# Kernel optimization log

Measured on AMD Instinct MI355X. Metric: run time of the kernel, lower is better.

Reference implementation:

```python
import jax, jax.numpy as jnp
import numpy as np

# ---- module hyperparameters (from init_kwargs) ----
DIST = 25
N_IN, N_HID, N_OUT = 16, 128, 2
D_MODEL, D_STATE, D_CONV, EXPAND, HEADDIM = 256, 64, 4, 2, 64
D_INNER = EXPAND * D_MODEL            # 512
NHEADS = D_INNER // HEADDIM           # 8
CONV_DIM = D_INNER + 2 * D_STATE      # 640 (x, B, C share the conv)
D_IN_PROJ = 2 * D_INNER + 2 * D_STATE + NHEADS  # 1160
NUM_CHECK = DIST ** 2 - 1             # 624 (mamba seq len)
NPG = NUM_CHECK + DIST ** 2           # 1249 nodes per graph
BATCH = 64
N_NODES = BATCH * NPG                 # 79936
N_EDGES = N_NODES * 8                 # 639488


def setup_inputs() -> dict:
    key = jax.random.key(0)
    ks = jax.random.split(key, 16)
    w = lambda k, shape, s=0.02: jax.random.normal(k, shape, jnp.float32) * s
    return {
        "node_inputs": jax.random.normal(ks[0], (N_NODES, N_IN), jnp.float32),
        "src_ids": jax.random.randint(ks[1], (N_EDGES,), 0, N_NODES),
        "dst_ids": jax.random.randint(ks[2], (N_EDGES,), 0, N_NODES),
        "W_embed": w(ks[3], (N_IN, D_MODEL)), "b_embed": jnp.zeros((D_MODEL,), jnp.float32),
        "W_in": w(ks[4], (D_MODEL, D_IN_PROJ)), "b_in": jnp.zeros((D_IN_PROJ,), jnp.float32),
        "conv_w": w(ks[5], (CONV_DIM, D_CONV), 0.1), "conv_b": jnp.zeros((CONV_DIM,), jnp.float32),
        "A_log": jnp.log(jnp.arange(1, NHEADS + 1, dtype=jnp.float32)),
        "dt_bias": w(ks[6], (NHEADS,), 0.1),
        "D_skip": jnp.ones((NHEADS,), jnp.float32),
        "norm_w": jnp.ones((D_INNER,), jnp.float32),
        "W_outp": w(ks[7], (D_INNER, D_MODEL)), "b_outp": jnp.zeros((D_MODEL,), jnp.float32),
        "W_proj": w(ks[8], (D_MODEL, N_IN)), "b_proj": jnp.zeros((N_IN,), jnp.float32),
        "W_msg": w(ks[9], (N_IN, N_HID)), "b_msg": jnp.zeros((N_HID,), jnp.float32),
        "W_upd": w(ks[10], (N_IN + N_HID, N_HID)), "b_upd": jnp.zeros((N_HID,), jnp.float32),
        "W_out": w(ks[11], (N_HID, N_OUT)), "b_out": jnp.zeros((N_OUT,), jnp.float32),
    }


def _silu(x):
    return x * jax.nn.sigmoid(x)


def _mamba2(x, W_in, b_in, conv_w, conv_b, A_log, dt_bias, D_skip, norm_w, W_outp, b_outp):
    """Mamba2 block: in_proj -> causal depthwise conv -> selective scan -> gated RMSNorm -> out_proj."""
    Bg, L, _ = x.shape
    zxbcdt = x @ W_in + b_in                       # [Bg, L, 1160]
    z = zxbcdt[..., :D_INNER]                      # gate
    xBC = zxbcdt[..., D_INNER:D_INNER + CONV_DIM]
    dt = zxbcdt[..., D_INNER + CONV_DIM:]          # [Bg, L, H]
    # causal depthwise conv over the seq dim (d_conv taps)
    xp = jnp.pad(xBC, ((0, 0), (D_CONV - 1, 0), (0, 0)))
    xBC = sum(conv_w[:, k] * xp[:, k:k + L, :] for k in range(D_CONV)) + conv_b
    xBC = _silu(xBC)
    xs = xBC[..., :D_INNER].reshape(Bg, L, NHEADS, HEADDIM)
    Bm = xBC[..., D_INNER:D_INNER + D_STATE]       # [Bg, L, N] (ngroups=1)
    Cm = xBC[..., D_INNER + D_STATE:]              # [Bg, L, N]
    dt = jax.nn.softplus(dt + dt_bias)             # [Bg, L, H]
    dA = jnp.exp(dt * (-jnp.exp(A_log)))           # [Bg, L, H]

    def step(h, inp):
        xt, Bt, Ct, dAt, dtt = inp                 # xt [Bg,H,P], Bt/Ct [Bg,N], dAt/dtt [Bg,H]
        h = dAt[..., None, None] * h + dtt[..., None, None] * xt[..., None] * Bt[:, None, None, :]
        yt = jnp.einsum('bhpn,bn->bhp', h, Ct)
        return h, yt

    h0 = jnp.zeros((Bg, NHEADS, HEADDIM, D_STATE), x.dtype)
    seq = (jnp.moveaxis(xs, 1, 0), jnp.moveaxis(Bm, 1, 0), jnp.moveaxis(Cm, 1, 0),
           jnp.moveaxis(dA, 1, 0), jnp.moveaxis(dt, 1, 0))
    _, ys = jax.lax.scan(step, h0, seq)
    ys = jnp.moveaxis(ys, 1, 0) + xs * D_skip[None, None, :, None]   # [Bg, L, H, P]
    y = ys.reshape(Bg, L, D_INNER) * _silu(z)                        # gated
    y = y * jax.lax.rsqrt(jnp.mean(y * y, axis=-1, keepdims=True) + 1e-5) * norm_w
    return y @ W_outp + b_outp


def reference(node_inputs, src_ids, dst_ids, W_embed, b_embed, W_in, b_in, conv_w, conv_b,
              A_log, dt_bias, D_skip, norm_w, W_outp, b_outp, W_proj, b_proj,
              W_msg, b_msg, W_upd, b_upd, W_out, b_out):
    # gather check-node rows: i*nodes_per_graph + j for j < num_check
    idx = (jnp.arange(BATCH)[:, None] * NPG + jnp.arange(NUM_CHECK)[None, :]).reshape(-1)
    chk = node_inputs[idx]                                           # [B*624, 16]
    emb = (chk @ W_embed + b_embed).reshape(BATCH, NUM_CHECK, D_MODEL)
    y = _mamba2(emb, W_in, b_in, conv_w, conv_b, A_log, dt_bias, D_skip, norm_w, W_outp, b_outp)
    proj = y.reshape(-1, D_MODEL) @ W_proj + b_proj                  # [B*624, 16]
    # scatter back into zero tensor at check-node slots
    feat = jnp.zeros((node_inputs.shape[0], N_IN), node_inputs.dtype).at[idx].set(proj)
    # GNN message passing: gather src, transform, scatter-sum into dst, update, readout
    msg = jax.nn.relu(feat[src_ids] @ W_msg + b_msg)                 # [E, n_hidden]
    agg = jax.ops.segment_sum(msg, dst_ids, num_segments=feat.shape[0])
    h = jax.nn.relu(jnp.concatenate([feat, agg], axis=-1) @ W_upd + b_upd)
    return h @ W_out + b_out                                         # [N, n_node_outputs]
```

## Files before the change

kernel.cpp:

```cpp
#include <hip/hip_runtime.h>
#include <math.h>

#define LSEQ 624
#define NPG_C 1249
#define BATCH_C 64
#define NROWS (BATCH_C*LSEQ)
#define N_NODES_C 79936
#define N_EDGES_C 639488
#define DIP 1160
#define DIN 512
#define CDIM 640
#define NH 8
#define HD 64
#define DS 64
#define CAP 96
#define TCH 48
#define NCHK 13
#define HSLOT 2097152

#define OFF_CHK   0
#define OFF_WF    638976
#define OFF_BF    657536
#define OFF_WOP   658944
#define OFF_BOP   667136
#define OFF_XBC   667392
#define OFF_DTV   26226432
#define OFF_EV    26545920
#define OFF_YS    26865408
#define OFF_FEAT  47312640
#define OFF_AGG   48591616
#define OFF_ECUM  (OFF_AGG + 2000000)
#define OFF_BBF   (OFF_AGG + 2400000)
#define OFF_PROJ  (OFF_XBC + 8000000)

typedef __attribute__((ext_vector_type(8))) short bf16x8;
typedef __attribute__((ext_vector_type(4))) float f32x4;

__device__ __forceinline__ float siluf(float x) {
    return x / (1.f + __expf(-x));
}

__device__ __forceinline__ unsigned short f2bf(float f) {
    unsigned int u = __float_as_uint(f);
    u += 0x7fffu + ((u >> 16) & 1u);
    return (unsigned short)(u >> 16);
}
__device__ __forceinline__ float bf2f(unsigned short h) {
    return __uint_as_float(((unsigned int)h) << 16);
}

__device__ __forceinline__ unsigned short* hstp(unsigned short* hst, int c, int b, int head) {
    return hst + (size_t)(c - 1) * HSLOT + (size_t)(b * NH + head) * 4096;
}

__global__ void k_gather(const float* __restrict__ ni, float* __restrict__ chk) {
    int gid = blockIdx.x * 256 + threadIdx.x;
    if (gid >= NROWS * 16) return;
    int row = gid >> 4, k = gid & 15;
    int node = (row / LSEQ) * NPG_C + (row % LSEQ);
    chk[gid] = ni[node * 16 + k];
}

__global__ void k_fusew(const float* __restrict__ We, const float* __restrict__ be,
                        const float* __restrict__ Wi, const float* __restrict__ bi,
                        const float* __restrict__ Wo, const float* __restrict__ bo,
                        const float* __restrict__ Wp, const float* __restrict__ bp,
                        float* __restrict__ Wf, float* __restrict__ bf,
                        float* __restrict__ Wop, float* __restrict__ bop) {
    int id = blockIdx.x * 256 + threadIdx.x;
    if (id < 16 * DIP) {
        int i = id / DIP, j = id % DIP;
        float s = 0.f;
        for (int k = 0; k < 256; k++) s = fmaf(We[i * 256 + k], Wi[k * DIP + j], s);
        Wf[id] = s;
    } else if (id < 16 * DIP + DIP) {
        int j = id - 16 * DIP;
        float s = bi[j];
        for (int k = 0; k < 256; k++) s = fmaf(be[k], Wi[k * DIP + j], s);
        bf[j] = s;
    } else if (id < 16 * DIP + DIP + DIN * 16) {
        int id2 = id - (16 * DIP + DIP);
        int c = id2 >> 4, o = id2 & 15;
        float s = 0.f;
        for (int k = 0; k < 256; k++) s = fmaf(Wo[c * 256 + k], Wp[k * 16 + o], s);
        Wop[id2] = s;
    } else if (id < 16 * DIP + DIP + DIN * 16 + 16) {
        int o = id - (16 * DIP + DIP + DIN * 16);
        float s = bp[o];
        for (int k = 0; k < 256; k++) s = fmaf(bo[k], Wp[k * 16 + o], s);
        bop[o] = s;
    }
}

__global__ __launch_bounds__(320) void k_conv(const float* __restrict__ chk,
        const float* __restrict__ Wf, const float* __restrict__ bf,
        const float* __restrict__ cw, const float* __restrict__ cb,
        float* __restrict__ xBCc, unsigned short* __restrict__ bbf) {
    int c = blockIdx.x * 320 + threadIdx.x;
    int t0 = blockIdx.y * 78;
    int b = blockIdx.z;
    float w[16];
#pragma unroll
    for (int k = 0; k < 16; k++) w[k] = Wf[k * DIP + DIN + c];
    float bfx = bf[DIN + c];
    float k0 = cw[c * 4 + 0], k1 = cw[c * 4 + 1], k2 = cw[c * 4 + 2], k3 = cw[c * 4 + 3];
    float cbv = cb[c];
    const float* crow = chk + (size_t)(b * LSEQ) * 16;
    float* out = xBCc + (size_t)(b * LSEQ) * CDIM + c;
    int isB = (c >= 512 && c < 576);
    unsigned short* bout = bbf + (size_t)(b * LSEQ) * 64 + (c - 512);

    float w0 = 0.f, w1 = 0.f, w2 = 0.f;
#pragma unroll
    for (int d = 3; d >= 1; d--) {
        int tau = t0 - d;
        float s = 0.f;
        if (tau >= 0) {
            s = bfx;
            const float* cr = crow + tau * 16;
#pragma unroll
            for (int k = 0; k < 16; k++) s = fmaf(cr[k], w[k], s);
        }
        if (d == 3) w0 = s; else if (d == 2) w1 = s; else w2 = s;
    }
    for (int t = t0; t < t0 + 78; t++) {
        const float* cr = crow + t * 16;
        float w3 = bfx;
#pragma unroll
        for (int k = 0; k < 16; k++) w3 = fmaf(cr[k], w[k], w3);
        float a = fmaf(k0, w0, fmaf(k1, w1, fmaf(k2, w2, fmaf(k3, w3, cbv))));
        float v = siluf(a);
        out[(size_t)t * CDIM] = v;
        if (isB) bout[(size_t)t * 64] = f2bf(v);
        w0 = w1; w1 = w2; w2 = w3;
    }
}

__global__ __launch_bounds__(256) void k_dte(const float* __restrict__ chk,
        const float* __restrict__ Wf, const float* __restrict__ bf,
        const float* __restrict__ A_log, const float* __restrict__ dt_bias,
        float* __restrict__ dtv, float* __restrict__ ecum) {
    int s = blockIdx.x * 4 + (threadIdx.x >> 6);
    int lane = threadIdx.x & 63;
    int h = s & 7;
    int cb = s >> 3;
    int c = cb % NCHK, b = cb / NCHK;
    int r0 = b * LSEQ + c * TCH;
    float wcol[16];
#pragma unroll
    for (int k = 0; k < 16; k++) wcol[k] = Wf[k * DIP + DIN + CDIM + h];
    float base = bf[DIN + CDIM + h] + dt_bias[h];
    float nA = -__expf(A_log[h]);
    float v = 0.f, sp = 0.f;
    if (lane < TCH) {
        const float* cr = chk + (size_t)(r0 + lane) * 16;
        float acc = base;
#pragma unroll
        for (int k = 0; k < 16; k++) acc = fmaf(cr[k], wcol[k], acc);
        sp = (acc > 20.f) ? acc : log1pf(__expf(acc));
        v = nA * sp;
    }
#pragma unroll
    for (int off = 1; off < 64; off <<= 1) {
        float u = __shfl_up(v, off);
        if (lane >= off) v += u;
    }
    if (lane < TCH) {
        dtv[(size_t)(r0 + lane) * NH + h] = sp;
        ecum[(size_t)(r0 + lane) * NH + h] = v;
    }
}

__global__ __launch_bounds__(256) void k_gmat(const float* __restrict__ xBCc,
        float* __restrict__ Gm) {
    int c = blockIdx.x, b = blockIdx.y;
    int tid = threadIdx.x;
    int bs = b * LSEQ;
    __shared__ __align__(16) float sBC[TCH * 132];
#pragma unroll
    for (int j = 0; j < 6; j++) {
        int g = j * 256 + tid;
        int f = g * 4;
        int t = f >> 7, col = f & 127;
        float4 v = *(const float4*)(xBCc + (size_t)(bs + c * TCH + t) * CDIM + 512 + col);
        *(float4*)&sBC[t * 132 + col] = v;
    }
    __syncthreads();
    int t0 = (tid >> 4) * 3, s0 = (tid & 15) * 3;
    float acc[3][3];
#pragma unroll
    for (int i = 0; i < 3; i++)
#pragma unroll
        for (int j = 0; j < 3; j++) acc[i][j] = 0.f;
    for (int k = 0; k < 64; k++) {
        float c0 = sBC[(t0 + 0) * 132 + 64 + k];
        float c1 = sBC[(t0 + 1) * 132 + 64 + k];
        float c2 = sBC[(t0 + 2) * 132 + 64 + k];
        float b0 = sBC[(s0 + 0) * 132 + k];
        float b1 = sBC[(s0 + 1) * 132 + k];
        float b2 = sBC[(s0 + 2) * 132 + k];
        acc[0][0] = fmaf(c0, b0, acc[0][0]); acc[0][1] = fmaf(c0, b1, acc[0][1]); acc[0][2] = fmaf(c0, b2, acc[0][2]);
        acc[1][0] = fmaf(c1, b0, acc[1][0]); acc[1][1] = fmaf(c1, b1, acc[1][1]); acc[1][2] = fmaf(c1, b2, acc[1][2]);
        acc[2][0] = fmaf(c2, b0, acc[2][0]); acc[2][1] = fmaf(c2, b1, acc[2][1]); acc[2][2] = fmaf(c2, b2, acc[2][2]);
    }
    size_t gb = (size_t)(b * NCHK + c) * (TCH * TCH);
#pragma unroll
    for (int i = 0; i < 3; i++)
#pragma unroll
        for (int j = 0; j < 3; j++)
            Gm[gb + (t0 + i) * TCH + (s0 + j)] = acc[i][j];
}

__global__ __launch_bounds__(256) void k_scarry(const float* __restrict__ xBCc,
        const unsigned short* __restrict__ bbf,
        const float* __restrict__ dtv, const float* __restrict__ ecum,
        unsigned short* __restrict__ hst) {
    int head = blockIdx.x, b = blockIdx.y;
    int pz = blockIdx.z * 32;
    int tid = threadIdx.x;
    int bs = b * LSEQ;
    __shared__ __align__(16) float sX[TCH * 32];
    __shared__ __align__(16) float sB[TCH * 64];
    __shared__ float sW[TCH];

    int i2 = (tid >> 4) * 2;
    int j4 = (tid & 15) * 4;

    float h[2][4];
#pragma unroll
    for (int i = 0; i < 2; i++)
#pragma unroll
        for (int j = 0; j < 4; j++) h[i][j] = 0.f;

    float4 rX0, rX1;
    ushort4 rBu[3];
    float rEc = 0.f, rDt = 0.f, rEcL = 0.f;

#define SC_ISSUE(cc)                                                                \
    {                                                                               \
        int r0i = bs + (cc) * TCH;                                                  \
        {   int f = 4 * tid; int t = f >> 5; int col = f & 31;                      \
            rX0 = *(const float4*)(xBCc + (size_t)(r0i + t) * CDIM + head * HD + pz + col); \
            if (tid < 128) {                                                        \
                int f2 = 1024 + 4 * tid; int t2 = f2 >> 5; int col2 = f2 & 31;      \
                rX1 = *(const float4*)(xBCc + (size_t)(r0i + t2) * CDIM + head * HD + pz + col2); \
            }                                                                       \
        }                                                                           \
        _Pragma("unroll")                                                           \
        for (int jj = 0; jj < 3; jj++) {                                            \
            int g = jj * 256 + tid; int f = 4 * g; int t = f >> 6; int col = f & 63;\
            rBu[jj] = *(const ushort4*)(bbf + (size_t)(r0i + t) * 64 + col);        \
        }                                                                           \
        if (tid < TCH) { rEc = ecum[(size_t)(r0i + tid) * NH + head];               \
                         rDt = dtv[(size_t)(r0i + tid) * NH + head]; }              \
        rEcL = ecum[(size_t)(r0i + TCH - 1) * NH + head];                           \
    }

    SC_ISSUE(0);
    for (int c = 0; c < NCHK; c++) {
        __syncthreads();
        float eL = __expf(rEcL);
        {
            int f = 4 * tid;
            *(float4*)&sX[f] = rX0;
            if (tid < 128) *(float4*)&sX[1024 + f] = rX1;
        }
#pragma unroll
        for (int jj = 0; jj < 3; jj++) {
            int g = jj * 256 + tid;
            float4 bv = { bf2f(rBu[jj].x), bf2f(rBu[jj].y), bf2f(rBu[jj].z), bf2f(rBu[jj].w) };
            *(float4*)&sB[4 * g] = bv;
        }
        if (tid < TCH) sW[tid] = __expf(rEcL - rEc) * rDt;
        __syncthreads();
        if (c + 1 < NCHK) SC_ISSUE(c + 1);

        if (c > 0) {
            unsigned short* hp = hstp(hst, c, b, head);
#pragma unroll
            for (int ii = 0; ii < 2; ii++) {
                ushort4 v = { f2bf(h[ii][0]), f2bf(h[ii][1]), f2bf(h[ii][2]), f2bf(h[ii][3]) };
                *(ushort4*)&hp[(pz + i2 + ii) * 64 + j4] = v;
            }
        }

#pragma unroll
        for (int i = 0; i < 2; i++)
#pragma unroll
            for (int j = 0; j < 4; j++) h[i][j] *= eL;
        for (int s = 0; s < TCH; s++) {
            float w = sW[s];
            float2 xv = *(const float2*)&sX[s * 32 + i2];
            float4 bv = *(const float4*)&sB[s * 64 + j4];
            float x0 = w * xv.x, x1 = w * xv.y;
            h[0][0] = fmaf(x0, bv.x, h[0][0]); h[0][1] = fmaf(x0, bv.y, h[0][1]);
            h[0][2] = fmaf(x0, bv.z, h[0][2]); h[0][3] = fmaf(x0, bv.w, h[0][3]);
            h[1][0] = fmaf(x1, bv.x, h[1][0]); h[1][1] = fmaf(x1, bv.y, h[1][1]);
            h[1][2] = fmaf(x1, bv.z, h[1][2]); h[1][3] = fmaf(x1, bv.w, h[1][3]);
        }
    }
#undef SC_ISSUE
}

__global__ __launch_bounds__(256) void k_intra(float* __restrict__ xBCc,
        const float* __restrict__ Gm, const float* __restrict__ dtv,
        const float* __restrict__ ecum, const float* __restrict__ Dskip,
        const unsigned short* __restrict__ hst) {
    int bid = blockIdx.x;
    int xcd = bid & 7;
    int head = (bid >> 3) & 7;
    int g = (bid >> 6) * 8 + xcd;
    int c = g % NCHK, b = g / NCHK;
    int tid = threadIdx.x;
    int lane = tid & 63;
    int wv = tid >> 6;
    int bs = b * LSEQ;
    int r0 = bs + c * TCH;

    __shared__ __align__(16) unsigned char smraw[52032];
    float* sXf = (float*)(smraw);
    unsigned short* sHt = (unsigned short*)(smraw);
    unsigned short* sCt = (unsigned short*)(smraw + 12288);
    unsigned short* sMh = (unsigned short*)(smraw + 19200);
    unsigned short* sMl = (unsigned short*)(smraw + 26112);
    unsigned short* sXh = (unsigned short*)(smraw + 33024);
    unsigned short* sXl = (unsigned short*)(smraw + 42240);
    float* sE  = (float*)(smraw + 51456);
    float* sEx = (float*)(smraw + 51648);
    float* sdt = (float*)(smraw + 51840);

    ushort4 rHu[4];
    if (c > 0) {
        const unsigned short* hp = hstp((unsigned short*)hst, c, b, head);
#pragma unroll
        for (int j = 0; j < 4; j++)
            rHu[j] = *(const ushort4*)(hp + 4 * (j * 256 + tid));
    }

#pragma unroll
    for (int j = 0; j < 3; j++) {
        int g2 = j * 256 + tid;
        int t = g2 >> 4, col = (g2 & 15) * 4;
        const float* rowp = xBCc + (size_t)(r0 + t) * CDIM;
        float4 xv = *(const float4*)(rowp + head * HD + col);
        *(float4*)&sXf[t * 64 + col] = xv;
        float4 cv = *(const float4*)(rowp + 576 + col);
        ushort4 cu = { f2bf(cv.x), f2bf(cv.y), f2bf(cv.z), f2bf(cv.w) };
        *(ushort4*)&sCt[t * 72 + col] = cu;
    }
    if (tid < TCH) {
        float e = ecum[(size_t)(r0 + tid) * NH + head];
        sE[tid] = e;
        sEx[tid] = __expf(e);
        sdt[tid] = dtv[(size_t)(r0 + tid) * NH + head];
    }
    __syncthreads();

    size_t gb = (size_t)(b * NCHK + c) * (TCH * TCH);
#pragma unroll
    for (int k = 0; k < 9; k++) {
        int id = k * 256 + tid;
        int t = id / TCH, s = id - t * TCH;
        float gv = Gm[gb + id];
        float m = (s <= t) ? __expf(sE[t] - sE[s]) * sdt[s] * gv : 0.f;
        unsigned short mh = f2bf(m);
        sMh[t * 72 + s] = mh;
        sMl[t * 72 + s] = f2bf(m - bf2f(mh));
    }
    for (int w = tid; w < 768; w += 256) {
        int t = w >> 4, s = 48 + (w & 15);
        sMh[t * 72 + s] = 0;
        sMl[t * 72 + s] = 0;
    }
#pragma unroll
    for (int i = 0; i < 3; i++) {
        int w = i * 256 + tid;
        int p = w & 63, k4 = (w >> 6) * 4;
        float v0 = sXf[(k4 + 0) * 64 + p];
        float v1 = sXf[(k4 + 1) * 64 + p];
        float v2 = sXf[(k4 + 2) * 64 + p];
        float v3 = sXf[(k4 + 3) * 64 + p];
        unsigned short h0 = f2bf(v0), h1 = f2bf(v1), h2 = f2bf(v2), h3 = f2bf(v3);
        ushort4 hi = { h0, h1, h2, h3 };
        ushort4 lo = { f2bf(v0 - bf2f(h0)), f2bf(v1 - bf2f(h1)),
                       f2bf(v2 - bf2f(h2)), f2bf(v3 - bf2f(h3)) };
        *(ushort4*)&sXh[p * 72 + k4] = hi;
        *(ushort4*)&sXl[p * 72 + k4] = lo;
    }
    {
        int p = tid >> 2, k4 = 48 + (tid & 3) * 4;
        ushort4 z = { 0, 0, 0, 0 };
        *(ushort4*)&sXh[p * 72 + k4] = z;
        *(ushort4*)&sXl[p * 72 + k4] = z;
    }
    __syncthreads();

    int pt = wv * 16;
    int colL = lane & 15;
    int rbase = (lane >> 4) * 4;
    int kfrag = 8 * (lane >> 4);

    float xo[3][4];
#pragma unroll
    for (int tt = 0; tt < 3; tt++)
#pragma unroll
        for (int r = 0; r < 4; r++)
            xo[tt][r] = sXf[(tt * 16 + rbase + r) * 64 + pt + colL];

    f32x4 acc[3] = { {0,0,0,0}, {0,0,0,0}, {0,0,0,0} };
    f32x4 acc2[3] = { {0,0,0,0}, {0,0,0,0}, {0,0,0,0} };
#pragma unroll
    for (int ks = 0; ks < 64; ks += 32) {
        bf16x8 bh = *(const bf16x8*)&sXh[(pt + colL) * 72 + ks + kfrag];
        bf16x8 bl = *(const bf16x8*)&sXl[(pt + colL) * 72 + ks + kfrag];
#pragma unroll
        for (int tt = 0; tt < 3; tt++) {
            bf16x8 ah = *(const bf16x8*)&sMh[(tt * 16 + colL) * 72 + ks + kfrag];
            bf16x8 al = *(const bf16x8*)&sMl[(tt * 16 + colL) * 72 + ks + kfrag];
            acc[tt] = __builtin_amdgcn_mfma_f32_16x16x32_bf16(ah, bh, acc[tt], 0, 0, 0);
            acc[tt] = __builtin_amdgcn_mfma_f32_16x16x32_bf16(ah, bl, acc[tt], 0, 0, 0);
            acc[tt] = __builtin_amdgcn_mfma_f32_16x16x32_bf16(al, bh, acc[tt], 0, 0, 0);
        }
    }
    __syncthreads();
    if (c > 0) {
#pragma unroll
        for (int j = 0; j < 4; j++) {
            int e = 4 * (j * 256 + tid);
            int p = e >> 6, n4 = e & 63;
            *(ushort4*)&sHt[p * 72 + n4] = rHu[j];
        }
    }
    __syncthreads();
    if (c > 0) {
#pragma unroll
        for (int ks = 0; ks < 64; ks += 32) {
            bf16x8 bhh = *(const bf16x8*)&sHt[(pt + colL) * 72 + ks + kfrag];
#pragma unroll
            for (int tt = 0; tt < 3; tt++) {
                bf16x8 ac = *(const bf16x8*)&sCt[(tt * 16 + colL) * 72 + ks + kfrag];
                acc2[tt] = __builtin_amdgcn_mfma_f32_16x16x32_bf16(ac, bhh, acc2[tt], 0, 0, 0);
            }
        }
    }

    float dsk = Dskip[head];
#pragma unroll
    for (int tt = 0; tt < 3; tt++) {
#pragma unroll
        for (int r = 0; r < 4; r++) {
            int trow = tt * 16 + rbase + r;
            float y = fmaf(dsk, xo[tt][r], acc[tt][r]);
            if (c > 0) y = fmaf(sEx[trow], acc2[tt][r], y);
            xBCc[(size_t)(r0 + trow) * CDIM + head * HD + pt + colL] = y;
        }
    }
}

__global__ __launch_bounds__(256) void k_gate(const float* __restrict__ chk,
        const float* __restrict__ Wf, const float* __restrict__ bf,
        const float* __restrict__ ysx, const float* __restrict__ norm_w,
        const float* __restrict__ Wop, const float* __restrict__ bop,
        float* __restrict__ feat) {
    int row0 = blockIdx.x * 8;
    int tid = threadIdx.x;
    __shared__ float sy[512];
    __shared__ float sred[256];
    __shared__ float swave[4];
    int c1 = tid, c2 = tid + 256;
    float wz1[16], wz2[16];
#pragma unroll
    for (int k = 0; k < 16; k++) {
        wz1[k] = Wf[k * DIP + c1];
        wz2[k] = Wf[k * DIP + c2];
    }
    float zb1 = bf[c1], zb2 = bf[c2];
    float nw1 = norm_w[c1], nw2 = norm_w[c2];
    int o = tid & 15, kg = tid >> 4;
    int wid = tid >> 6, lane = tid & 63;
    for (int r = 0; r < 8; r++) {
        int row = row0 + r;
        const float4* cp = (const float4*)(chk + (size_t)row * 16);
        float4 cA = cp[0], cB = cp[1], cC = cp[2], cD = cp[3];
        float cv[16] = {cA.x,cA.y,cA.z,cA.w, cB.x,cB.y,cB.z,cB.w,
                        cC.x,cC.y,cC.z,cC.w, cD.x,cD.y,cD.z,cD.w};
        float z1 = zb1, z2 = zb2;
#pragma unroll
        for (int k = 0; k < 16; k++) {
            z1 = fmaf(cv[k], wz1[k], z1);
            z2 = fmaf(cv[k], wz2[k], z2);
        }
        float y1 = ysx[(size_t)row * CDIM + c1] * siluf(z1);
        float y2 = ysx[(size_t)row * CDIM + c2] * siluf(z2);
        float ss = y1 * y1 + y2 * y2;
#pragma unroll
        for (int off = 32; off >= 1; off >>= 1) ss += __shfl_xor(ss, off);
        if (lane == 0) swave[wid] = ss;
        __syncthreads();
        float tot = swave[0] + swave[1] + swave[2] + swave[3];
        float scale = 1.f / sqrtf(tot * (1.f / 512.f) + 1e-5f);
        sy[c1] = y1 * scale * nw1;
        sy[c2] = y2 * scale * nw2;
        __syncthreads();
        float ps = 0.f;
#pragma unroll
        for (int j = 0; j < 32; j++) {
            int k = kg * 32 + j;
            ps = fmaf(sy[k], Wop[k * 16 + o], ps);
        }
        sred[kg * 16 + o] = ps;
        __syncthreads();
        if (tid < 16) {
            float s = bop[tid];
#pragma unroll
            for (int g = 0; g < 16; g++) s += sred[g * 16 + tid];
            int bb = row / LSEQ, t = row % LSEQ;
            feat[(size_t)(bb * NPG_C + t) * 16 + tid] = s;
        }
    }
}

__global__ void k_scatter(const int* __restrict__ src, const int* __restrict__ dst,
                          int* __restrict__ cnt, int* __restrict__ slots) {
    int e = blockIdx.x * 256 + threadIdx.x;
    if (e >= N_EDGES_C) return;
    int d = dst[e];
    int pos = atomicAdd(&cnt[d], 1);
    if (pos < CAP) slots[(size_t)d * CAP + pos] = src[e];
}

__global__ __launch_bounds__(256) void k_proj(const float* __restrict__ feat,
        const float* __restrict__ Wm, const float* __restrict__ bm,
        unsigned short* __restrict__ p) {
    int tid = threadIdx.x;
    int c = tid & 127, half = tid >> 7;
    float w[16];
#pragma unroll
    for (int k = 0; k < 16; k++) w[k] = Wm[k * 128 + c];
    float bmv = bm[c];
    int base = blockIdx.x * 8;
#pragma unroll
    for (int q = 0; q < 4; q++) {
        int node = base + q * 2 + half;
        const float4* fr = (const float4*)(feat + (size_t)node * 16);
        float4 f0 = fr[0], f1 = fr[1], f2 = fr[2], f3 = fr[3];
        float m = bmv;
        m = fmaf(f0.x, w[0],  m); m = fmaf(f0.y, w[1],  m);
        m = fmaf(f0.z, w[2],  m); m = fmaf(f0.w, w[3],  m);
        m = fmaf(f1.x, w[4],  m); m = fmaf(f1.y, w[5],  m);
        m = fmaf(f1.z, w[6],  m); m = fmaf(f1.w, w[7],  m);
        m = fmaf(f2.x, w[8],  m); m = fmaf(f2.y, w[9],  m);
        m = fmaf(f2.z, w[10], m); m = fmaf(f2.w, w[11], m);
        m = fmaf(f3.x, w[12], m); m = fmaf(f3.y, w[13], m);
        m = fmaf(f3.z, w[14], m); m = fmaf(f3.w, w[15], m);
        p[(size_t)node * 128 + c] = f2bf(fmaxf(m, 0.f));
    }
}

__global__ __launch_bounds__(256) void k_agg2(const int* __restrict__ cnt,
        const int* __restrict__ slots, const unsigned short* __restrict__ p,
        float* __restrict__ agg) {
    int wid = threadIdx.x >> 6, lane = threadIdx.x & 63;
    int esub = lane >> 4, cl = lane & 15;
    int d = blockIdx.x * 4 + wid;
    int deg = cnt[d];
    if (deg > CAP) deg = CAP;
    const int* sl = slots + (size_t)d * CAP;

    float acc[8];
#pragma unroll
    for (int j = 0; j < 8; j++) acc[j] = 0.f;

    int e = esub;
    int s = (e < deg) ? sl[e] : -1;
    while (e < deg) {
        int scur = s;
        int en = e + 4;
        if (en < deg) s = sl[en];
        ushort4 v0, v1;
        {
            const unsigned short* pp = p + (size_t)scur * 128 + cl * 8;
            v0 = *(const ushort4*)(pp);
            v1 = *(const ushort4*)(pp + 4);
        }
        acc[0] += bf2f(v0.x); acc[1] += bf2f(v0.y);
        acc[2] += bf2f(v0.z); acc[3] += bf2f(v0.w);
        acc[4] += bf2f(v1.x); acc[5] += bf2f(v1.y);
        acc[6] += bf2f(v1.z); acc[7] += bf2f(v1.w);
        e = en;
    }
#pragma unroll
    for (int j = 0; j < 8; j++) {
        acc[j] += __shfl_xor(acc[j], 16);
        acc[j] += __shfl_xor(acc[j], 32);
    }
    if (esub == 0) {
        float4 o0 = { acc[0], acc[1], acc[2], acc[3] };
        float4 o1 = { acc[4], acc[5], acc[6], acc[7] };
        float* ap = agg + (size_t)d * 128 + cl * 8;
        *(float4*)(ap) = o0;
        *(float4*)(ap + 4) = o1;
    }
}

#define UNB 32
__global__ __launch_bounds__(256) void k_upd2(const float* __restrict__ feat,
        const float* __restrict__ agg, const float* __restrict__ Wu,
        const float* __restrict__ bu, const float* __restrict__ Wo2,
        const float* __restrict__ bo2, float* __restrict__ out) {
    int g0 = blockIdx.x * UNB;
    int tid = threadIdx.x;
    __shared__ __align__(16) float sin_[UNB][144];
    __shared__ float part[4][8][2];
    for (int w = tid; w < UNB * 144; w += 256) {
        int node = w / 144, k = w - node * 144;
        sin_[node][k] = (k < 16) ? feat[(size_t)(g0 + node) * 16 + k]
                                 : agg[(size_t)(g0 + node) * 128 + (k - 16)];
    }
    __syncthreads();
    int c6 = tid & 63;
    int grp = tid >> 6;
    float acc[8][2];
#pragma unroll
    for (int nn = 0; nn < 8; nn++) { acc[nn][0] = 0.f; acc[nn][1] = 0.f; }

    for (int k0 = 0; k0 < 144; k0 += 4) {
        float wA0 = Wu[(k0 + 0) * 128 + c6], wB0 = Wu[(k0 + 0) * 128 + 64 + c6];
        float wA1 = Wu[(k0 + 1) * 128 + c6], wB1 = Wu[(k0 + 1) * 128 + 64 + c6];
        float wA2 = Wu[(k0 + 2) * 128 + c6], wB2 = Wu[(k0 + 2) * 128 + 64 + c6];
        float wA3 = Wu[(k0 + 3) * 128 + c6], wB3 = Wu[(k0 + 3) * 128 + 64 + c6];
#pragma unroll
        for (int nn = 0; nn < 8; nn++) {
            float4 s4 = *(const float4*)&sin_[grp * 8 + nn][k0];
            acc[nn][0] = fmaf(s4.x, wA0, acc[nn][0]);
            acc[nn][1] = fmaf(s4.x, wB0, acc[nn][1]);
            acc[nn][0] = fmaf(s4.y, wA1, acc[nn][0]);
            acc[nn][1] = fmaf(s4.y, wB1, acc[nn][1]);
            acc[nn][0] = fmaf(s4.z, wA2, acc[nn][0]);
            acc[nn][1] = fmaf(s4.z, wB2, acc[nn][1]);
            acc[nn][0] = fmaf(s4.w, wA3, acc[nn][0]);
            acc[nn][1] = fmaf(s4.w, wB3, acc[nn][1]);
        }
    }

    float buA = bu[c6], buB = bu[64 + c6];
    float2 woA = *(const float2*)&Wo2[c6 * 2];
    float2 woB = *(const float2*)&Wo2[(64 + c6) * 2];
    float p[8][2];
#pragma unroll
    for (int nn = 0; nn < 8; nn++) {
        float h0 = fmaxf(acc[nn][0] + buA, 0.f);
        float h1 = fmaxf(acc[nn][1] + buB, 0.f);
        p[nn][0] = h0 * woA.x + h1 * woB.x;
        p[nn][1] = h0 * woA.y + h1 * woB.y;
    }
#pragma unroll
    for (int off = 1; off < 64; off <<= 1) {
#pragma unroll
        for (int nn = 0; nn < 8; nn++) {
            p[nn][0] += __shfl_xor(p[nn][0], off);
            p[nn][1] += __shfl_xor(p[nn][1], off);
        }
    }
    if ((tid & 63) == 0) {
#pragma unroll
        for (int nn = 0; nn < 8; nn++) {
            part[grp][nn][0] = p[nn][0];
            part[grp][nn][1] = p[nn][1];
        }
    }
    __syncthreads();
    if (tid < 64) {
        int node = tid >> 1, o = tid & 1;
        out[(size_t)(g0 + node) * 2 + o] = part[node >> 3][node & 7][o] + bo2[o];
    }
}

extern "C" void kernel_launch(void* const* d_in, const int* in_sizes, int n_in,
                              void* d_out, int out_size, void* d_ws, size_t ws_size,
                              hipStream_t stream) {
    const float* node_inputs = (const float*)d_in[0];
    const int*   src_ids     = (const int*)d_in[1];
    const int*   dst_ids     = (const int*)d_in[2];
    const float* W_embed     = (const float*)d_in[3];
    const float* b_embed     = (const float*)d_in[4];
    const float* W_in        = (const float*)d_in[5];
    const float* b_in        = (const float*)d_in[6];
    const float* conv_w      = (const float*)d_in[7];
    const float* conv_b      = (const float*)d_in[8];
    const float* A_log       = (const float*)d_in[9];
    const float* dt_bias     = (const float*)d_in[10];
    const float* D_skip      = (const float*)d_in[11];
    const float* norm_w      = (const float*)d_in[12];
    const float* W_outp      = (const float*)d_in[13];
    const float* b_outp      = (const float*)d_in[14];
    const float* W_proj      = (const float*)d_in[15];
    const float* b_proj      = (const float*)d_in[16];
    const float* W_msg       = (const float*)d_in[17];
    const float* b_msg       = (const float*)d_in[18];
    const float* W_upd       = (const float*)d_in[19];
    const float* b_upd       = (const float*)d_in[20];
    const float* W_out       = (const float*)d_in[21];
    const float* b_out       = (const float*)d_in[22];

    float* ws   = (float*)d_ws;
    float* chk  = ws + OFF_CHK;
    float* Wf   = ws + OFF_WF;
    float* bf   = ws + OFF_BF;
    float* Wop  = ws + OFF_WOP;
    float* bop  = ws + OFF_BOP;
    float* xBCc = ws + OFF_XBC;
    float* dtv  = ws + OFF_DTV;
    float* ecum = ws + OFF_ECUM;
    unsigned short* hst = (unsigned short*)(ws + OFF_YS);
    unsigned short* bbf = (unsigned short*)(ws + OFF_BBF);
    float* feat = ws + OFF_FEAT;
    float* agg  = ws + OFF_AGG;
    float* Gm   = ws + OFF_AGG;
    unsigned short* pmsg = (unsigned short*)(ws + OFF_PROJ);
    int*   slots = (int*)(ws + OFF_XBC);
    int*   cnt   = (int*)(ws + OFF_DTV);
    float* out  = (float*)d_out;

    hipMemsetAsync(feat, 0, (size_t)N_NODES_C * 16 * 4, stream);

    k_gather<<<(NROWS * 16 + 255) / 256, 256, 0, stream>>>(node_inputs, chk);
    k_fusew<<<(16 * DIP + DIP + DIN * 16 + 16 + 255) / 256, 256, 0, stream>>>(
        W_embed, b_embed, W_in, b_in, W_outp, b_outp, W_proj, b_proj, Wf, bf, Wop, bop);
    k_conv<<<dim3(2, 8, BATCH_C), 320, 0, stream>>>(chk, Wf, bf, conv_w, conv_b, xBCc, bbf);
    k_dte<<<(BATCH_C * NCHK * NH) / 4, 256, 0, stream>>>(chk, Wf, bf, A_log, dt_bias, dtv, ecum);
    k_gmat<<<dim3(NCHK, BATCH_C), 256, 0, stream>>>(xBCc, Gm);
    k_scarry<<<dim3(NH, BATCH_C, 2), 256, 0, stream>>>(xBCc, bbf, dtv, ecum, hst);
    k_intra<<<NCHK * NH * BATCH_C, 256, 0, stream>>>(xBCc, Gm, dtv, ecum, D_skip, hst);
    k_gate<<<NROWS / 8, 256, 0, stream>>>(chk, Wf, bf, xBCc, norm_w, Wop, bop, feat);
    hipMemsetAsync(cnt, 0, (size_t)N_NODES_C * 4, stream);
    k_scatter<<<(N_EDGES_C + 255) / 256, 256, 0, stream>>>(src_ids, dst_ids, cnt, slots);
    k_proj<<<N_NODES_C / 8, 256, 0, stream>>>(feat, W_msg, b_msg, pmsg);
    k_agg2<<<N_NODES_C / 4, 256, 0, stream>>>(cnt, slots, pmsg, agg);
    k_upd2<<<N_NODES_C / UNB, 256, 0, stream>>>(feat, agg, W_upd, b_upd, W_out, b_out, out);
}
```

Before: 409.8 us.

## Drop X low-split MFMA in intra-chunk and rewrite gate as wave-per-row kernel

In k_intra, the X operand's bf16 low-part split is removed, leaving two of the three MFMAs per tile. Shared memory is shrunk by aliasing the C and H tiles onto buffers that are already dead, with C held in registers until late, which may allow more resident blocks. k_gate is rewritten so each wave handles one row with bf16 weights cached in LDS, a shuffle-only RMSNorm and a butterfly transpose-reduction, removing the per-row block barriers. Both changes lower precision: X and the gate/out-proj weights are rounded to bf16.

```diff
diff --git a/kernel.cpp b/kernel.cpp
--- a/kernel.cpp
+++ b/kernel.cpp
@@ -34,6 +34,7 @@
 #define OFF_PROJ  (OFF_XBC + 8000000)
 
 typedef __attribute__((ext_vector_type(8))) short bf16x8;
+typedef __attribute__((ext_vector_type(8))) unsigned short u16x8;
 typedef __attribute__((ext_vector_type(4))) float f32x4;
 
 __device__ __forceinline__ float siluf(float x) {
@@ -317,17 +318,16 @@
     int bs = b * LSEQ;
     int r0 = bs + c * TCH;
 
-    __shared__ __align__(16) unsigned char smraw[52032];
+    __shared__ __align__(16) unsigned char smraw[35904];
     float* sXf = (float*)(smraw);
-    unsigned short* sHt = (unsigned short*)(smraw);
-    unsigned short* sCt = (unsigned short*)(smraw + 12288);
-    unsigned short* sMh = (unsigned short*)(smraw + 19200);
-    unsigned short* sMl = (unsigned short*)(smraw + 26112);
-    unsigned short* sXh = (unsigned short*)(smraw + 33024);
-    unsigned short* sXl = (unsigned short*)(smraw + 42240);
-    float* sE  = (float*)(smraw + 51456);
-    float* sEx = (float*)(smraw + 51648);
-    float* sdt = (float*)(smraw + 51840);
+    unsigned short* sMh = (unsigned short*)(smraw + 12288);
+    unsigned short* sMl = (unsigned short*)(smraw + 19200);
+    unsigned short* sCt = (unsigned short*)(smraw + 19200);
+    unsigned short* sXh = (unsigned short*)(smraw + 26112);
+    unsigned short* sHt = (unsigned short*)(smraw + 26112);
+    float* sE  = (float*)(smraw + 35328);
+    float* sEx = (float*)(smraw + 35520);
+    float* sdt = (float*)(smraw + 35712);
 
     ushort4 rHu[4];
     if (c > 0) {
@@ -337,6 +337,7 @@
             rHu[j] = *(const ushort4*)(hp + 4 * (j * 256 + tid));
     }
 
+    ushort4 rCu[3];
 #pragma unroll
     for (int j = 0; j < 3; j++) {
         int g2 = j * 256 + tid;
@@ -346,7 +347,7 @@
         *(float4*)&sXf[t * 64 + col] = xv;
         float4 cv = *(const float4*)(rowp + 576 + col);
         ushort4 cu = { f2bf(cv.x), f2bf(cv.y), f2bf(cv.z), f2bf(cv.w) };
-        *(ushort4*)&sCt[t * 72 + col] = cu;
+        rCu[j] = cu;
     }
     if (tid < TCH) {
         float e = ecum[(size_t)(r0 + tid) * NH + head];
@@ -380,18 +381,13 @@
         float v1 = sXf[(k4 + 1) * 64 + p];
         float v2 = sXf[(k4 + 2) * 64 + p];
         float v3 = sXf[(k4 + 3) * 64 + p];
-        unsigned short h0 = f2bf(v0), h1 = f2bf(v1), h2 = f2bf(v2), h3 = f2bf(v3);
-        ushort4 hi = { h0, h1, h2, h3 };
-        ushort4 lo = { f2bf(v0 - bf2f(h0)), f2bf(v1 - bf2f(h1)),
-                       f2bf(v2 - bf2f(h2)), f2bf(v3 - bf2f(h3)) };
+        ushort4 hi = { f2bf(v0), f2bf(v1), f2bf(v2), f2bf(v3) };
         *(ushort4*)&sXh[p * 72 + k4] = hi;
-        *(ushort4*)&sXl[p * 72 + k4] = lo;
     }
     {
         int p = tid >> 2, k4 = 48 + (tid & 3) * 4;
         ushort4 z = { 0, 0, 0, 0 };
         *(ushort4*)&sXh[p * 72 + k4] = z;
-        *(ushort4*)&sXl[p * 72 + k4] = z;
     }
     __syncthreads();
 
@@ -412,17 +408,21 @@
 #pragma unroll
     for (int ks = 0; ks < 64; ks += 32) {
         bf16x8 bh = *(const bf16x8*)&sXh[(pt + colL) * 72 + ks + kfrag];
-        bf16x8 bl = *(const bf16x8*)&sXl[(pt + colL) * 72 + ks + kfrag];
 #pragma unroll
         for (int tt = 0; tt < 3; tt++) {
             bf16x8 ah = *(const bf16x8*)&sMh[(tt * 16 + colL) * 72 + ks + kfrag];
             bf16x8 al = *(const bf16x8*)&sMl[(tt * 16 + colL) * 72 + ks + kfrag];
             acc[tt] = __builtin_amdgcn_mfma_f32_16x16x32_bf16(ah, bh, acc[tt], 0, 0, 0);
-            acc[tt] = __builtin_amdgcn_mfma_f32_16x16x32_bf16(ah, bl, acc[tt], 0, 0, 0);
             acc[tt] = __builtin_amdgcn_mfma_f32_16x16x32_bf16(al, bh, acc[tt], 0, 0, 0);
         }
     }
     __syncthreads();
+#pragma unroll
+    for (int j = 0; j < 3; j++) {
+        int g2 = j * 256 + tid;
+        int t = g2 >> 4, col = (g2 & 15) * 4;
+        *(ushort4*)&sCt[t * 72 + col] = rCu[j];
+    }
     if (c > 0) {
 #pragma unroll
         for (int j = 0; j < 4; j++) {
@@ -457,65 +457,109 @@
     }
 }
 
-__global__ __launch_bounds__(256) void k_gate(const float* __restrict__ chk,
+#define GROWS 16
+__global__ __launch_bounds__(256) void k_gate2(const float* __restrict__ chk,
         const float* __restrict__ Wf, const float* __restrict__ bf,
         const float* __restrict__ ysx, const float* __restrict__ norm_w,
         const float* __restrict__ Wop, const float* __restrict__ bop,
         float* __restrict__ feat) {
-    int row0 = blockIdx.x * 8;
+    __shared__ unsigned short sWz[16 * 512];
+    __shared__ unsigned short sWo[16 * 512];
     int tid = threadIdx.x;
-    __shared__ float sy[512];
-    __shared__ float sred[256];
-    __shared__ float swave[4];
-    int c1 = tid, c2 = tid + 256;
-    float wz1[16], wz2[16];
-#pragma unroll
-    for (int k = 0; k < 16; k++) {
-        wz1[k] = Wf[k * DIP + c1];
-        wz2[k] = Wf[k * DIP + c2];
-    }
-    float zb1 = bf[c1], zb2 = bf[c2];
-    float nw1 = norm_w[c1], nw2 = norm_w[c2];
-    int o = tid & 15, kg = tid >> 4;
-    int wid = tid >> 6, lane = tid & 63;
-    for (int r = 0; r < 8; r++) {
-        int row = row0 + r;
+    for (int i = tid; i < 8192; i += 256) {
+        int k = i >> 9, cc = i & 511;
+        sWz[i] = f2bf(Wf[k * DIP + cc]);
+        sWo[i] = f2bf(Wop[cc * 16 + k]);
+    }
+    __syncthreads();
+    int lane = tid & 63, wv = tid >> 6;
+    int c8 = lane * 8;
+    float4 zb0 = *(const float4*)&bf[c8];
+    float4 zb1 = *(const float4*)&bf[c8 + 4];
+    float4 nw0 = *(const float4*)&norm_w[c8];
+    float4 nw1 = *(const float4*)&norm_w[c8 + 4];
+    int olane = ((lane >> 5) & 1) * 8 + ((lane >> 4) & 1) * 4
+              + ((lane >> 3) & 1) * 2 + ((lane >> 2) & 1);
+    float bop_o = bop[olane];
+
+    for (int rr = 0; rr < GROWS / 4; rr++) {
+        int row = blockIdx.x * GROWS + wv + rr * 4;
         const float4* cp = (const float4*)(chk + (size_t)row * 16);
         float4 cA = cp[0], cB = cp[1], cC = cp[2], cD = cp[3];
         float cv[16] = {cA.x,cA.y,cA.z,cA.w, cB.x,cB.y,cB.z,cB.w,
                         cC.x,cC.y,cC.z,cC.w, cD.x,cD.y,cD.z,cD.w};
-        float z1 = zb1, z2 = zb2;
+        float z[8] = {zb0.x, zb0.y, zb0.z, zb0.w, zb1.x, zb1.y, zb1.z, zb1.w};
 #pragma unroll
         for (int k = 0; k < 16; k++) {
-            z1 = fmaf(cv[k], wz1[k], z1);
-            z2 = fmaf(cv[k], wz2[k], z2);
-        }
-        float y1 = ysx[(size_t)row * CDIM + c1] * siluf(z1);
-        float y2 = ysx[(size_t)row * CDIM + c2] * siluf(z2);
-        float ss = y1 * y1 + y2 * y2;
-#pragma unroll
-        for (int off = 32; off >= 1; off >>= 1) ss += __shfl_xor(ss, off);
-        if (lane == 0) swave[wid] = ss;
-        __syncthreads();
-        float tot = swave[0] + swave[1] + swave[2] + swave[3];
-        float scale = 1.f / sqrtf(tot * (1.f / 512.f) + 1e-5f);
-        sy[c1] = y1 * scale * nw1;
-        sy[c2] = y2 * scale * nw2;
-        __syncthreads();
-        float ps = 0.f;
-#pragma unroll
-        for (int j = 0; j < 32; j++) {
-            int k = kg * 32 + j;
-            ps = fmaf(sy[k], Wop[k * 16 + o], ps);
-        }
-        sred[kg * 16 + o] = ps;
-        __syncthreads();
-        if (tid < 16) {
-            float s = bop[tid];
-#pragma unroll
-            for (int g = 0; g < 16; g++) s += sred[g * 16 + tid];
+            u16x8 wz = *(const u16x8*)&sWz[k * 512 + c8];
+            float ck = cv[k];
+#pragma unroll
+            for (int j = 0; j < 8; j++)
+                z[j] = fmaf(ck, bf2f((unsigned short)wz[j]), z[j]);
+        }
+        float4 y0 = *(const float4*)&ysx[(size_t)row * CDIM + c8];
+        float4 y1 = *(const float4*)&ysx[(size_t)row * CDIM + c8 + 4];
+        float yv[8] = {y0.x, y0.y, y0.z, y0.w, y1.x, y1.y, y1.z, y1.w};
+        float gn[8];
+        float ss = 0.f;
+#pragma unroll
+        for (int j = 0; j < 8; j++) {
+            gn[j] = yv[j] * siluf(z[j]);
+            ss = fmaf(gn[j], gn[j], ss);
+        }
+#pragma unroll
+        for (int off = 1; off < 64; off <<= 1) ss += __shfl_xor(ss, off);
+        float scale = 1.f / sqrtf(ss * (1.f / 512.f) + 1e-5f);
+        float nwv[8] = {nw0.x, nw0.y, nw0.z, nw0.w, nw1.x, nw1.y, nw1.z, nw1.w};
+#pragma unroll
+        for (int j = 0; j < 8; j++) gn[j] *= scale * nwv[j];
+
+        float p[16];
+#pragma unroll
+        for (int o = 0; o < 16; o++) {
+            u16x8 wo = *(const u16x8*)&sWo[o * 512 + c8];
+            float s = 0.f;
+#pragma unroll
+            for (int j = 0; j < 8; j++)
+                s = fmaf(gn[j], bf2f((unsigned short)wo[j]), s);
+            p[o] = s;
+        }
+        bool b5 = (lane & 32) != 0;
+        float s8[8];
+#pragma unroll
+        for (int j = 0; j < 8; j++) {
+            float sel = b5 ? p[j + 8] : p[j];
+            float oth = b5 ? p[j] : p[j + 8];
+            s8[j] = sel + __shfl_xor(oth, 32);
+        }
+        bool b4 = (lane & 16) != 0;
+        float s4[4];
+#pragma unroll
+        for (int j = 0; j < 4; j++) {
+            float sel = b4 ? s8[j + 4] : s8[j];
+            float oth = b4 ? s8[j] : s8[j + 4];
+            s4[j] = sel + __shfl_xor(oth, 16);
+        }
+        bool b3 = (lane & 8) != 0;
+        float s2[2];
+#pragma unroll
+        for (int j = 0; j < 2; j++) {
+            float sel = b3 ? s4[j + 2] : s4[j];
+            float oth = b3 ? s4[j] : s4[j + 2];
+            s2[j] = sel + __shfl_xor(oth, 8);
+        }
+        bool b2 = (lane & 4) != 0;
+        float s1;
+        {
+            float sel = b2 ? s2[1] : s2[0];
+            float oth = b2 ? s2[0] : s2[1];
+            s1 = sel + __shfl_xor(oth, 4);
+        }
+        s1 += __shfl_xor(s1, 2);
+        s1 += __shfl_xor(s1, 1);
+        if ((lane & 3) == 0) {
             int bb = row / LSEQ, t = row % LSEQ;
-            feat[(size_t)(bb * NPG_C + t) * 16 + tid] = s;
+            feat[(size_t)(bb * NPG_C + t) * 16 + olane] = s1 + bop_o;
         }
     }
 }
@@ -732,7 +776,7 @@
     k_gmat<<<dim3(NCHK, BATCH_C), 256, 0, stream>>>(xBCc, Gm);
     k_scarry<<<dim3(NH, BATCH_C, 2), 256, 0, stream>>>(xBCc, bbf, dtv, ecum, hst);
     k_intra<<<NCHK * NH * BATCH_C, 256, 0, stream>>>(xBCc, Gm, dtv, ecum, D_skip, hst);
-    k_gate<<<NROWS / 8, 256, 0, stream>>>(chk, Wf, bf, xBCc, norm_w, Wop, bop, feat);
+    k_gate2<<<NROWS / GROWS, 256, 0, stream>>>(chk, Wf, bf, xBCc, norm_w, Wop, bop, feat);
     hipMemsetAsync(cnt, 0, (size_t)N_NODES_C * 4, stream);
     k_scatter<<<(N_EDGES_C + 255) / 256, 256, 0, stream>>>(src_ids, dst_ids, cnt, slots);
     k_proj<<<N_NODES_C / 8, 256, 0, stream>>>(feat, W_msg, b_msg, pmsg);
```

Result: slower. 488.3 us (+19.2%).
